# Kernel optimization log

Hardware: AMD Instinct MI355X
Metric: run time of the kernel (lower is better)

## Reference

```python
import jax, jax.numpy as jnp
import numpy as np

B, LQ, LK = 4, 4096, 4096
D = 1024          # num_heads * key_dim = 16 * 64
Q_DIM = 1024      # query_dim
K_DIM = 1024      # note: linear_k input dim; here inputs carry d_model features
V_DIM = 1024      # value_dim


def setup_inputs() -> dict:
    key = jax.random.key(0)
    ks = jax.random.split(key, 12)
    s_in = 1.0 / np.sqrt(Q_DIM)
    s_d = 1.0 / np.sqrt(D)
    return {
        "q": jax.random.normal(ks[0], (B, LQ, Q_DIM), jnp.float32),
        "k": jax.random.normal(ks[1], (B, LK, K_DIM), jnp.float32),
        "v": jax.random.normal(ks[2], (B, LK, V_DIM), jnp.float32),
        # Linear weights stored [in, out] so projection is x @ W + b
        "Wq": jax.random.normal(ks[3], (Q_DIM, D), jnp.float32) * s_in,
        "bq": jax.random.normal(ks[4], (D,), jnp.float32) * s_in,
        "Wk": jax.random.normal(ks[5], (K_DIM, D), jnp.float32) * s_in,
        "bk": jax.random.normal(ks[6], (D,), jnp.float32) * s_in,
        "Wv": jax.random.normal(ks[7], (V_DIM, D), jnp.float32) * s_in,
        "bv": jax.random.normal(ks[8], (D,), jnp.float32) * s_in,
        "Wo": jax.random.normal(ks[9], (D, V_DIM), jnp.float32) * s_d,
        "bo": jax.random.normal(ks[10], (V_DIM,), jnp.float32) * s_d,
    }


def reference(q, k, v, Wq, bq, Wk, bk, Wv, bv, Wo, bo):
    # Projections: [B, L, D]
    qp = jax.nn.softmax(q @ Wq + bq, axis=-1)   # softmax over feature dim
    kp = jax.nn.softmax(k @ Wk + bk, axis=-2)   # softmax over sequence dim
    vp = jax.nn.softmax(v @ Wv + bv, axis=-2)   # softmax over sequence dim
    # Dropout is identity in eval mode (module uses dropout_p at train only).
    scores = jnp.einsum("bqd,bkd->bqk", qp, kp)  # [B, LQ, LK]
    ctx = jnp.einsum("bqk,bkd->bqd", scores, vp)  # [B, LQ, D]
    return ctx @ Wo + bo                          # [B, LQ, V_DIM]
```

## Files before the change

kernel.cpp:

```cpp
#include <hip/hip_runtime.h>

typedef _Float16 f16x8 __attribute__((ext_vector_type(8)));
typedef float f32x4 __attribute__((ext_vector_type(4)));
typedef long lx2 __attribute__((ext_vector_type(2)));

__device__ __forceinline__ float h2f(unsigned short h) {
  return (float)__builtin_bit_cast(_Float16, h);
}
__device__ __forceinline__ unsigned short f2h(float f) {
  return __builtin_bit_cast(unsigned short, (_Float16)f);
}

#if __has_builtin(__builtin_amdgcn_cvt_pk_fp8_f32)
#define HW_FP8 1
#else
#define HW_FP8 0
#endif

__device__ __forceinline__ unsigned char f2e4_sw(float f) {
  unsigned short h = __builtin_bit_cast(unsigned short, (_Float16)f);
  unsigned s = (h >> 8) & 0x80u;
  unsigned ae = h & 0x7FFFu;
  if (ae >= 0x5F00u) return (unsigned char)(s | 0x7Eu);
  if (ae >= 0x2400u) {
    unsigned t = ae - 0x2000u;
    t = (t + 0x3Fu + ((t >> 7) & 1u)) >> 7;
    return (unsigned char)(s | t);
  }
  float v = (float)__builtin_bit_cast(_Float16, (unsigned short)ae) * 512.0f;
  int n = (int)rintf(v);
  return (unsigned char)(s | (unsigned)n);
}

__device__ __forceinline__ unsigned pk2e4(float a, float b) {
#if HW_FP8
  return (unsigned)__builtin_amdgcn_cvt_pk_fp8_f32(a, b, 0, false) & 0xFFFFu;
#else
  return (unsigned)f2e4_sw(a) | ((unsigned)f2e4_sw(b) << 8);
#endif
}
__device__ __forceinline__ unsigned pk4e4(float a, float b, float c, float d) {
#if HW_FP8
  int lo = __builtin_amdgcn_cvt_pk_fp8_f32(a, b, 0, false);
  return (unsigned)__builtin_amdgcn_cvt_pk_fp8_f32(c, d, lo, true);
#else
  return (unsigned)f2e4_sw(a) | ((unsigned)f2e4_sw(b) << 8) |
         ((unsigned)f2e4_sw(c) << 16) | ((unsigned)f2e4_sw(d) << 24);
#endif
}

__device__ __forceinline__ void gload_lds16(const void* g, void* l) {
  __builtin_amdgcn_global_load_lds(
      (const __attribute__((address_space(1))) void*)g,
      (__attribute__((address_space(3))) void*)l, 16, 0, 0);
}

__global__ __launch_bounds__(512, 4) void proj3(
    const float* __restrict__ A0, const float* __restrict__ A1,
    const float* __restrict__ A2, const unsigned short* __restrict__ WTb,
    const float* __restrict__ b0, const float* __restrict__ b1,
    const float* __restrict__ b2, unsigned char* __restrict__ C0,
    unsigned char* __restrict__ C1, unsigned char* __restrict__ C2,
    float* __restrict__ s0, float* __restrict__ s1, float* __restrict__ s2)
{
  __shared__ alignas(16) unsigned char smem[49152];
  const int tid  = threadIdx.x;
  const int lane = tid & 63;
  const int wave = tid >> 6;
  const int waveM = wave >> 2;
  const int waveN = wave & 3;

  const int wg = (int)blockIdx.x;
  const int w  = (wg & 7) * 192 + (wg >> 3);
  const int z  = w / 512;
  const int wl = w - z * 512;
  const int x  = wl & 3;
  const int rem = wl >> 2;
  const int y  = rem & 31;
  const int bz = rem >> 5;

  const float* Af = (z == 0) ? A0 : (z == 1) ? A1 : A2;
  const float* bi = (z == 0) ? b0 : (z == 1) ? b1 : b2;
  unsigned char* Cp = (z == 0) ? C0 : (z == 1) ? C1 : C2;
  float* sums = (z == 0) ? s0 : (z == 1) ? s1 : s2;

  const int m0 = y * 128, n0 = x * 256;

  const int srow = tid >> 3;
  const int scol = ((tid * 16) & 127) ^ ((srow & 7) << 4);
  const char* BpR = (const char*)(WTb + (size_t)z * 1048576)
                    + (size_t)n0 * 2048 + (size_t)srow * 2048 + scol;
  const char* ApR32 = (const char*)Af + (size_t)bz * (4096L * 1024 * 4)
                      + (size_t)m0 * 4096 + (size_t)srow * 4096 + (size_t)scol * 2;
  const unsigned oA0 = (unsigned)tid * 16;

  int offA[4], offB[4];
  {
    const int q16 = (lane >> 4) << 4;
#pragma unroll
    for (int mi = 0; mi < 4; ++mi) {
      const int r = waveM * 64 + mi * 16 + (lane & 15);
      offA[mi] = r * 128 + (q16 ^ ((r & 7) << 4));
    }
#pragma unroll
    for (int ni = 0; ni < 4; ++ni) {
      const int r = waveN * 64 + ni * 16 + (lane & 15);
      offB[ni] = 16384 + r * 128 + (q16 ^ ((r & 7) << 4));
    }
  }

  f32x4 acc[4][4] = {};

  float4 pf0, pf1, pf2, pf3;
  {
    const char* sa = ApR32;
    const char* sb = sa + 4096 * 64;
    pf0 = *(const float4*)sa;  pf1 = *(const float4*)(sa + 16);
    pf2 = *(const float4*)sb;  pf3 = *(const float4*)(sb + 16);
  }

  for (int kt = 0; kt < 16; ++kt) {
    const size_t kb = (size_t)kt * 128;
    {
      unsigned short h0[8], h1[8];
      const float* fa0 = (const float*)&pf0; const float* fa1 = (const float*)&pf1;
      const float* fb0 = (const float*)&pf2; const float* fb1 = (const float*)&pf3;
#pragma unroll
      for (int e = 0; e < 4; ++e) {
        h0[e] = f2h(fa0[e]); h0[4 + e] = f2h(fa1[e]);
        h1[e] = f2h(fb0[e]); h1[4 + e] = f2h(fb1[e]);
      }
      *(uint4*)&smem[oA0]        = *(const uint4*)h0;
      *(uint4*)&smem[oA0 + 8192] = *(const uint4*)h1;
      if (kt + 1 < 16) {
        const char* sa = ApR32 + (size_t)(kt + 1) * 256;
        const char* sb = sa + 4096 * 64;
        pf0 = *(const float4*)sa;  pf1 = *(const float4*)(sa + 16);
        pf2 = *(const float4*)sb;  pf3 = *(const float4*)(sb + 16);
      }
    }
    gload_lds16(BpR + kb,                      smem + 16384 + oA0);
    gload_lds16(BpR + 2048 * 64 + kb,          smem + 16384 + oA0 + 8192);
    gload_lds16(BpR + 2048 * 128 + kb,         smem + 16384 + oA0 + 16384);
    gload_lds16(BpR + 2048 * 192 + kb,         smem + 16384 + oA0 + 24576);
    __syncthreads();
#pragma unroll
    for (int kk = 0; kk < 2; ++kk) {
      const int kx = kk << 6;
      f16x8 aF[4], bF[4];
#pragma unroll
      for (int mi = 0; mi < 4; ++mi) aF[mi] = *(const f16x8*)&smem[offA[mi] ^ kx];
#pragma unroll
      for (int ni = 0; ni < 4; ++ni) bF[ni] = *(const f16x8*)&smem[offB[ni] ^ kx];
#pragma unroll
      for (int mi = 0; mi < 4; ++mi)
#pragma unroll
        for (int ni = 0; ni < 4; ++ni)
          acc[mi][ni] = __builtin_amdgcn_mfma_f32_16x16x32_f16(aF[mi], bF[ni], acc[mi][ni], 0, 0, 0);
    }
    __syncthreads();
  }

  const int rb = (lane >> 4) * 4;
  const int cb_ = lane & 15;
  const long sC = 4096L * 1024;

  if (z == 0) {
#pragma unroll
    for (int m = 0; m < 4; ++m) {
      const int row0 = m0 + waveM * 64 + m * 16 + rb;
      float rs0 = 0, rs1 = 0, rs2 = 0, rs3 = 0;
#pragma unroll
      for (int n = 0; n < 4; ++n) {
        const int col = n0 + waveN * 64 + n * 16 + cb_;
        const float badd = bi[col];
        const float e0 = __expf(acc[m][n][0] + badd);
        const float e1 = __expf(acc[m][n][1] + badd);
        const float e2 = __expf(acc[m][n][2] + badd);
        const float e3 = __expf(acc[m][n][3] + badd);
        const unsigned p01 = pk2e4(e0 * 0.0625f, e1 * 0.0625f);
        const unsigned p23 = pk2e4(e2 * 0.0625f, e3 * 0.0625f);
        unsigned char* C8 = Cp + (long)bz * sC;
        C8[(size_t)(row0 + 0) * 1024 + col] = (unsigned char)(p01 & 0xff);
        C8[(size_t)(row0 + 1) * 1024 + col] = (unsigned char)((p01 >> 8) & 0xff);
        C8[(size_t)(row0 + 2) * 1024 + col] = (unsigned char)(p23 & 0xff);
        C8[(size_t)(row0 + 3) * 1024 + col] = (unsigned char)((p23 >> 8) & 0xff);
        rs0 += e0; rs1 += e1; rs2 += e2; rs3 += e3;
      }
#pragma unroll
      for (int off = 1; off <= 8; off <<= 1) {
        rs0 += __shfl_xor(rs0, off);
        rs1 += __shfl_xor(rs1, off);
        rs2 += __shfl_xor(rs2, off);
        rs3 += __shfl_xor(rs3, off);
      }
      if ((lane & 15) == 0) {
        float* s = sums + (size_t)bz * 4096 + row0;
        atomicAdd(s + 0, rs0);
        atomicAdd(s + 1, rs1);
        atomicAdd(s + 2, rs2);
        atomicAdd(s + 3, rs3);
      }
    }
  } else {
    float cs[4] = {0.f, 0.f, 0.f, 0.f};
#pragma unroll
    for (int m = 0; m < 4; ++m) {
      const int row0 = m0 + waveM * 64 + m * 16 + rb;
#pragma unroll
      for (int n = 0; n < 4; ++n) {
        const int col = n0 + waveN * 64 + n * 16 + cb_;
        const float badd = bi[col];
        float ev[4];
        float ls = 0.f;
#pragma unroll
        for (int r = 0; r < 4; ++r) {
          ev[r] = __expf(acc[m][n][r] + badd);
          ls += ev[r];
        }
        cs[n] += ls;
        *(unsigned*)(Cp + (long)bz * sC + ((size_t)col << 12) + row0) =
            pk4e4(ev[0] * 0.0625f, ev[1] * 0.0625f, ev[2] * 0.0625f, ev[3] * 0.0625f);
      }
    }
#pragma unroll
    for (int n = 0; n < 4; ++n) {
      cs[n] += __shfl_xor(cs[n], 16);
      cs[n] += __shfl_xor(cs[n], 32);
    }
    if (lane < 16) {
#pragma unroll
      for (int n = 0; n < 4; ++n) {
        const int col = n0 + waveN * 64 + n * 16 + lane;
        atomicAdd(sums + ((size_t)bz << 10) + col, cs[n]);
      }
    }
  }
}

template <int OUTMODE>
__global__ __launch_bounds__(512, 4) void gemm8(
    const unsigned char* __restrict__ A, const unsigned char* __restrict__ Bt,
    void* __restrict__ Cv, const float* __restrict__ bias,
    const float* __restrict__ sums,
    int N, int K, int ldk, int gx, int gy, int nsplit,
    long sA, long sB, long sC)
{
  __shared__ alignas(16) unsigned char smem[49152];
  const int tid  = threadIdx.x;
  const int lane = tid & 63;
  const int wave = tid >> 6;
  const int waveM = wave >> 2;
  const int waveN = wave & 3;

  const int nwg = (int)gridDim.x;
  const int cpx = nwg >> 3;
  const int wg  = (int)blockIdx.x;
  const int w   = (wg & 7) * cpx + (wg >> 3);
  const int x   = w % gx;
  const int rem = w / gx;
  const int y   = rem % gy;
  const int zt  = rem / gy;
  const int bz  = zt / nsplit;
  const int sp  = zt % nsplit;

  const int m0 = y * 128, n0 = x * 256;
  const size_t ldkB = (size_t)ldk;
  const size_t ldkB64 = ldkB * 64, ldkB128 = ldkB * 128;

  const int srow = tid >> 3;
  const int scol = ((tid * 16) & 127) ^ ((srow & 7) << 4);
  const char* ApR;
  const char* BpR;
  {
    const char* Ab = (const char*)A + (long)bz * sA + (long)sp * K + (size_t)m0 * ldkB;
    const char* Bb = (const char*)Bt + (long)bz * sB + (long)sp * K + (size_t)n0 * ldkB;
    ApR = Ab + (size_t)srow * ldkB + scol;
    BpR = Bb + (size_t)srow * ldkB + scol;
  }
  const unsigned oA0 = (unsigned)tid * 16;

  int offA[4], offB[4];
  {
    const int q16 = (lane >> 4) << 4;
#pragma unroll
    for (int mi = 0; mi < 4; ++mi) {
      const int r = waveM * 64 + mi * 16 + (lane & 15);
      offA[mi] = r * 128 + (q16 ^ ((r & 7) << 4));
    }
#pragma unroll
    for (int ni = 0; ni < 4; ++ni) {
      const int r = waveN * 64 + ni * 16 + (lane & 15);
      offB[ni] = 16384 + r * 128 + (q16 ^ ((r & 7) << 4));
    }
  }

  f32x4 acc[4][4] = {};

  const int nk = K >> 7;
  for (int kt = 0; kt < nk; ++kt) {
    const size_t kb = (size_t)kt * 128;
    gload_lds16(ApR + kb,                     smem + oA0);
    gload_lds16(ApR + ldkB64 + kb,            smem + oA0 + 8192);
    gload_lds16(BpR + kb,                     smem + 16384 + oA0);
    gload_lds16(BpR + ldkB64 + kb,            smem + 16384 + oA0 + 8192);
    gload_lds16(BpR + ldkB128 + kb,           smem + 16384 + oA0 + 16384);
    gload_lds16(BpR + ldkB128 + ldkB64 + kb,  smem + 16384 + oA0 + 24576);
    __syncthreads();
#pragma unroll
    for (int kk = 0; kk < 2; ++kk) {
      const int kx = kk << 6;
      lx2 aF[4], bF[4];
#pragma unroll
      for (int mi = 0; mi < 4; ++mi) aF[mi] = *(const lx2*)&smem[offA[mi] ^ kx];
#pragma unroll
      for (int ni = 0; ni < 4; ++ni) bF[ni] = *(const lx2*)&smem[offB[ni] ^ kx];
#pragma unroll
      for (int h = 0; h < 2; ++h)
#pragma unroll
        for (int mi = 0; mi < 4; ++mi)
#pragma unroll
          for (int ni = 0; ni < 4; ++ni)
            acc[mi][ni] = __builtin_amdgcn_mfma_f32_16x16x32_fp8_fp8(
                aF[mi][h], bF[ni][h], acc[mi][ni], 0, 0, 0);
    }
    __syncthreads();
  }

  const int rb = (lane >> 4) * 4;
  const int cb_ = lane & 15;
  const long zout = (OUTMODE == 2) ? (long)zt : (long)bz;
#pragma unroll
  for (int m = 0; m < 4; ++m) {
    const int row0 = m0 + waveM * 64 + m * 16 + rb;
    float i0 = 0, i1 = 0, i2 = 0, i3 = 0;
    if (OUTMODE == 5) {
      const float4 s4 = *(const float4*)&sums[(size_t)zout * 4096 + row0];
      i0 = 1.0f / (256.0f * s4.x); i1 = 1.0f / (256.0f * s4.y);
      i2 = 1.0f / (256.0f * s4.z); i3 = 1.0f / (256.0f * s4.w);
    }
#pragma unroll
    for (int n = 0; n < 4; ++n) {
      const int col = n0 + waveN * 64 + n * 16 + cb_;
      if (OUTMODE == 2) {
#pragma unroll
        for (int r = 0; r < 4; ++r)
          ((unsigned short*)Cv)[zout * sC + (size_t)(row0 + r) * N + col] = f2h(acc[m][n][r]);
      } else {
        const float badd = bias[col];
        float* C32 = (float*)Cv;
        C32[zout * sC + (size_t)(row0 + 0) * N + col] = acc[m][n][0] * i0 + badd;
        C32[zout * sC + (size_t)(row0 + 1) * N + col] = acc[m][n][1] * i1 + badd;
        C32[zout * sC + (size_t)(row0 + 2) * N + col] = acc[m][n][2] * i2 + badd;
        C32[zout * sC + (size_t)(row0 + 3) * N + col] = acc[m][n][3] * i3 + badd;
      }
    }
  }
}

__global__ __launch_bounds__(256) void w_trh4(
    const float* __restrict__ W0, const float* __restrict__ W1,
    const float* __restrict__ W2, const float* __restrict__ W3,
    unsigned short* __restrict__ WTb, unsigned char* __restrict__ WoT8)
{
  __shared__ unsigned short tile[64][73];
  const int z = blockIdx.z;
  const float* W = (z == 0) ? W0 : (z == 1) ? W1 : (z == 2) ? W2 : W3;
  unsigned short* WT = WTb + (size_t)z * 1024 * 1024;
  const int c0 = blockIdx.x * 64;
  const int r0 = blockIdx.y * 64;
  const int tid = threadIdx.x;
  const int r = tid >> 2;
  const int cq = (tid & 3) * 16;
#pragma unroll
  for (int i = 0; i < 4; ++i) {
    const int c = cq + i * 4;
    const float4 v = *(const float4*)&W[(size_t)(r0 + r) * 1024 + c0 + c];
    tile[r][c + 0] = f2h(v.x);
    tile[r][c + 1] = f2h(v.y);
    tile[r][c + 2] = f2h(v.z);
    tile[r][c + 3] = f2h(v.w);
  }
  __syncthreads();
  const int c = tid >> 2;
  const int rq = (tid & 3) * 16;
  unsigned short outv[16];
#pragma unroll
  for (int j = 0; j < 16; ++j) outv[j] = tile[rq + j][c];
  unsigned short* Tb = WT + (size_t)(c0 + c) * 1024 + r0 + rq;
  ((uint4*)Tb)[0] = ((const uint4*)outv)[0];
  ((uint4*)Tb)[1] = ((const uint4*)outv)[1];
  if (z == 3) {
    unsigned u4[4];
#pragma unroll
    for (int j = 0; j < 4; ++j)
      u4[j] = pk4e4(h2f(outv[4 * j + 0]) * 8.f, h2f(outv[4 * j + 1]) * 8.f,
                    h2f(outv[4 * j + 2]) * 8.f, h2f(outv[4 * j + 3]) * 8.f);
    *(uint4*)(WoT8 + (size_t)(c0 + c) * 1024 + r0 + rq) = *(const uint4*)u4;
  }
}

__global__ __launch_bounds__(256) void red4m(
    const unsigned short* __restrict__ P, const float* __restrict__ skr,
    const float* __restrict__ svr, unsigned char* __restrict__ O)
{
  const int i = blockIdx.x * 256 + threadIdx.x;
  const int b = i >> 18;
  const int j = i & 262143;
  const int dk = j >> 8;
  const int dv0 = (j & 255) << 2;
  float s0 = 0, s1 = 0, s2 = 0, s3 = 0;
#pragma unroll
  for (int sl = 0; sl < 4; ++sl) {
    const uint2 u = *(const uint2*)(P + (((long)(b * 4 + sl)) << 20) + ((long)j << 2));
    s0 += h2f(u.x & 0xffff); s1 += h2f(u.x >> 16);
    s2 += h2f(u.y & 0xffff); s3 += h2f(u.y >> 16);
  }
  const float fk = 4194304.0f / skr[(b << 10) + dk];
  const float4 fv = *(const float4*)&svr[(b << 10) + dv0];
  ((unsigned*)O)[i] = pk4e4(s0 * fk / fv.x, s1 * fk / fv.y,
                            s2 * fk / fv.z, s3 * fk / fv.w);
}

__global__ __launch_bounds__(256) void red4g(
    const unsigned short* __restrict__ P, unsigned char* __restrict__ O)
{
  const int i = blockIdx.x * 256 + threadIdx.x;
  const int b = i >> 18;
  const int j = i & 262143;
  float s0 = 0, s1 = 0, s2 = 0, s3 = 0;
#pragma unroll
  for (int sl = 0; sl < 4; ++sl) {
    const uint2 u = *(const uint2*)(P + (((long)(b * 4 + sl)) << 20) + ((long)j << 2));
    s0 += h2f(u.x & 0xffff); s1 += h2f(u.x >> 16);
    s2 += h2f(u.y & 0xffff); s3 += h2f(u.y >> 16);
  }
  ((unsigned*)O)[i] = pk4e4(s0 * 0.03125f, s1 * 0.03125f,
                            s2 * 0.03125f, s3 * 0.03125f);
}

extern "C" void kernel_launch(void* const* d_in, const int* in_sizes, int n_in,
                              void* d_out, int out_size, void* d_ws, size_t ws_size,
                              hipStream_t stream) {
  const float* q  = (const float*)d_in[0];
  const float* k  = (const float*)d_in[1];
  const float* v  = (const float*)d_in[2];
  const float* Wq = (const float*)d_in[3];
  const float* bq = (const float*)d_in[4];
  const float* Wk = (const float*)d_in[5];
  const float* bk = (const float*)d_in[6];
  const float* Wv = (const float*)d_in[7];
  const float* bv = (const float*)d_in[8];
  const float* Wo = (const float*)d_in[9];
  const float* bo = (const float*)d_in[10];
  float* out = (float*)d_out;

  char* p = (char*)d_ws;
  unsigned short* Part = (unsigned short*)p; p += 33554432;
  unsigned short* WTb  = (unsigned short*)p; p += 8388608;
  unsigned char* WoT8 = (unsigned char*)p;   p += 1048576;
  unsigned char* Eq8  = (unsigned char*)p;   p += 16777216;
  unsigned char* ETk8 = (unsigned char*)p;   p += 16777216;
  unsigned char* ETv8 = (unsigned char*)p;   p += 16777216;
  unsigned char* Mh8  = (unsigned char*)p;   p += 4194304;
  unsigned char* GT8  = (unsigned char*)p;   p += 4194304;
  float* sqraw = (float*)p; p += 16384 * 4;
  float* skraw = (float*)p; p += 4096 * 4;
  float* svraw = (float*)p; p += 4096 * 4;

  const dim3 blk(256);
  const dim3 blk512(512);
  const long S22 = 4096L * 1024;
  const long S20 = 1024L * 1024;

  hipMemsetAsync(sqraw, 0, (16384 + 4096 + 4096) * sizeof(float), stream);

  w_trh4<<<dim3(16, 16, 4), blk, 0, stream>>>(Wq, Wk, Wv, Wo, WTb, WoT8);

  proj3<<<1536, blk512, 0, stream>>>(q, k, v, WTb, bq, bk, bv,
                                     Eq8, ETk8, ETv8, sqraw, skraw, svraw);

  gemm8<2><<<512, blk512, 0, stream>>>(ETk8, ETv8, Part, nullptr, nullptr,
      1024, 1024, 4096, 4, 8, 4, S22, S22, S20);
  red4m<<<4096, blk, 0, stream>>>(Part, skraw, svraw, Mh8);

  gemm8<2><<<512, blk512, 0, stream>>>(WoT8, Mh8, Part, nullptr, nullptr,
      1024, 256, 1024, 4, 8, 4, 0, S20, S20);
  red4g<<<4096, blk, 0, stream>>>(Part, GT8);

  gemm8<5><<<512, blk512, 0, stream>>>(Eq8, GT8, out, bo, sqraw,
      1024, 1024, 1024, 4, 32, 1, S22, S20, S22);

  (void)in_sizes; (void)n_in; (void)out_size; (void)ws_size;
}
```

Baseline: 263.0 us.

## Switch projection GEMM inputs and weights from fp16 to fp8 MFMA

The projection kernel now converts the fp32 activations and the transposed weights to fp8 e4m3, with the weights prescaled by 8. It runs fp8 MFMA over half as many K-tiles of 128 bytes, and the epilogue rescales the accumulator by 1/8. The weight-transpose kernel now writes one fp8 buffer for all four weights, which halves weight traffic and drops the separate fp16 copy. This cuts LDS and global bytes and doubles MFMA throughput per byte, at the cost of lower precision in the projection before the softmax.

```diff
diff --git a/kernel.cpp b/kernel.cpp
--- a/kernel.cpp
+++ b/kernel.cpp
@@ -1,6 +1,5 @@
 #include <hip/hip_runtime.h>
 
-typedef _Float16 f16x8 __attribute__((ext_vector_type(8)));
 typedef float f32x4 __attribute__((ext_vector_type(4)));
 typedef long lx2 __attribute__((ext_vector_type(2)));
 
@@ -32,13 +31,6 @@
   return (unsigned char)(s | (unsigned)n);
 }
 
-__device__ __forceinline__ unsigned pk2e4(float a, float b) {
-#if HW_FP8
-  return (unsigned)__builtin_amdgcn_cvt_pk_fp8_f32(a, b, 0, false) & 0xFFFFu;
-#else
-  return (unsigned)f2e4_sw(a) | ((unsigned)f2e4_sw(b) << 8);
-#endif
-}
 __device__ __forceinline__ unsigned pk4e4(float a, float b, float c, float d) {
 #if HW_FP8
   int lo = __builtin_amdgcn_cvt_pk_fp8_f32(a, b, 0, false);
@@ -48,6 +40,13 @@
          ((unsigned)f2e4_sw(c) << 16) | ((unsigned)f2e4_sw(d) << 24);
 #endif
 }
+__device__ __forceinline__ unsigned pk2e4(float a, float b) {
+#if HW_FP8
+  return (unsigned)__builtin_amdgcn_cvt_pk_fp8_f32(a, b, 0, false) & 0xFFFFu;
+#else
+  return (unsigned)f2e4_sw(a) | ((unsigned)f2e4_sw(b) << 8);
+#endif
+}
 
 __device__ __forceinline__ void gload_lds16(const void* g, void* l) {
   __builtin_amdgcn_global_load_lds(
@@ -57,7 +56,7 @@
 
 __global__ __launch_bounds__(512, 4) void proj3(
     const float* __restrict__ A0, const float* __restrict__ A1,
-    const float* __restrict__ A2, const unsigned short* __restrict__ WTb,
+    const float* __restrict__ A2, const unsigned char* __restrict__ WT8b,
     const float* __restrict__ b0, const float* __restrict__ b1,
     const float* __restrict__ b2, unsigned char* __restrict__ C0,
     unsigned char* __restrict__ C1, unsigned char* __restrict__ C2,
@@ -88,10 +87,10 @@
 
   const int srow = tid >> 3;
   const int scol = ((tid * 16) & 127) ^ ((srow & 7) << 4);
-  const char* BpR = (const char*)(WTb + (size_t)z * 1048576)
-                    + (size_t)n0 * 2048 + (size_t)srow * 2048 + scol;
-  const char* ApR32 = (const char*)Af + (size_t)bz * (4096L * 1024 * 4)
-                      + (size_t)m0 * 4096 + (size_t)srow * 4096 + (size_t)scol * 2;
+  const unsigned char* BpR = WT8b + ((size_t)z << 20)
+                             + (size_t)(n0 + srow) * 1024 + scol;
+  const float* ApR = Af + (size_t)bz * (4096L * 1024)
+                     + (size_t)(m0 + srow) * 1024 + scol;
   const unsigned oA0 = (unsigned)tid * 16;
 
   int offA[4], offB[4];
@@ -111,52 +110,54 @@
 
   f32x4 acc[4][4] = {};
 
-  float4 pf0, pf1, pf2, pf3;
-  {
-    const char* sa = ApR32;
-    const char* sb = sa + 4096 * 64;
-    pf0 = *(const float4*)sa;  pf1 = *(const float4*)(sa + 16);
-    pf2 = *(const float4*)sb;  pf3 = *(const float4*)(sb + 16);
-  }
-
-  for (int kt = 0; kt < 16; ++kt) {
+  float4 pa[4], pb[4];
+#pragma unroll
+  for (int j = 0; j < 4; ++j) {
+    pa[j] = *(const float4*)(ApR + j * 4);
+    pb[j] = *(const float4*)(ApR + 64 * 1024 + j * 4);
+  }
+
+  for (int kt = 0; kt < 8; ++kt) {
+    {
+      unsigned ua[4], ub[4];
+#pragma unroll
+      for (int j = 0; j < 4; ++j) {
+        ua[j] = pk4e4(pa[j].x, pa[j].y, pa[j].z, pa[j].w);
+        ub[j] = pk4e4(pb[j].x, pb[j].y, pb[j].z, pb[j].w);
+      }
+      *(uint4*)&smem[oA0]        = *(const uint4*)ua;
+      *(uint4*)&smem[oA0 + 8192] = *(const uint4*)ub;
+      if (kt + 1 < 8) {
+        const float* s = ApR + (size_t)(kt + 1) * 128;
+#pragma unroll
+        for (int j = 0; j < 4; ++j) {
+          pa[j] = *(const float4*)(s + j * 4);
+          pb[j] = *(const float4*)(s + 64 * 1024 + j * 4);
+        }
+      }
+    }
     const size_t kb = (size_t)kt * 128;
-    {
-      unsigned short h0[8], h1[8];
-      const float* fa0 = (const float*)&pf0; const float* fa1 = (const float*)&pf1;
-      const float* fb0 = (const float*)&pf2; const float* fb1 = (const float*)&pf3;
-#pragma unroll
-      for (int e = 0; e < 4; ++e) {
-        h0[e] = f2h(fa0[e]); h0[4 + e] = f2h(fa1[e]);
-        h1[e] = f2h(fb0[e]); h1[4 + e] = f2h(fb1[e]);
-      }
-      *(uint4*)&smem[oA0]        = *(const uint4*)h0;
-      *(uint4*)&smem[oA0 + 8192] = *(const uint4*)h1;
-      if (kt + 1 < 16) {
-        const char* sa = ApR32 + (size_t)(kt + 1) * 256;
-        const char* sb = sa + 4096 * 64;
-        pf0 = *(const float4*)sa;  pf1 = *(const float4*)(sa + 16);
-        pf2 = *(const float4*)sb;  pf3 = *(const float4*)(sb + 16);
-      }
-    }
-    gload_lds16(BpR + kb,                      smem + 16384 + oA0);
-    gload_lds16(BpR + 2048 * 64 + kb,          smem + 16384 + oA0 + 8192);
-    gload_lds16(BpR + 2048 * 128 + kb,         smem + 16384 + oA0 + 16384);
-    gload_lds16(BpR + 2048 * 192 + kb,         smem + 16384 + oA0 + 24576);
+    gload_lds16(BpR + kb,              smem + 16384 + oA0);
+    gload_lds16(BpR + 64 * 1024 + kb,  smem + 16384 + oA0 + 8192);
+    gload_lds16(BpR + 128 * 1024 + kb, smem + 16384 + oA0 + 16384);
+    gload_lds16(BpR + 192 * 1024 + kb, smem + 16384 + oA0 + 24576);
     __syncthreads();
 #pragma unroll
     for (int kk = 0; kk < 2; ++kk) {
       const int kx = kk << 6;
-      f16x8 aF[4], bF[4];
-#pragma unroll
-      for (int mi = 0; mi < 4; ++mi) aF[mi] = *(const f16x8*)&smem[offA[mi] ^ kx];
-#pragma unroll
-      for (int ni = 0; ni < 4; ++ni) bF[ni] = *(const f16x8*)&smem[offB[ni] ^ kx];
-#pragma unroll
-      for (int mi = 0; mi < 4; ++mi)
-#pragma unroll
-        for (int ni = 0; ni < 4; ++ni)
-          acc[mi][ni] = __builtin_amdgcn_mfma_f32_16x16x32_f16(aF[mi], bF[ni], acc[mi][ni], 0, 0, 0);
+      lx2 aF[4], bF[4];
+#pragma unroll
+      for (int mi = 0; mi < 4; ++mi) aF[mi] = *(const lx2*)&smem[offA[mi] ^ kx];
+#pragma unroll
+      for (int ni = 0; ni < 4; ++ni) bF[ni] = *(const lx2*)&smem[offB[ni] ^ kx];
+#pragma unroll
+      for (int h = 0; h < 2; ++h)
+#pragma unroll
+        for (int mi = 0; mi < 4; ++mi)
+#pragma unroll
+          for (int ni = 0; ni < 4; ++ni)
+            acc[mi][ni] = __builtin_amdgcn_mfma_f32_16x16x32_fp8_fp8(
+                aF[mi][h], bF[ni][h], acc[mi][ni], 0, 0, 0);
     }
     __syncthreads();
   }
@@ -174,10 +175,10 @@
       for (int n = 0; n < 4; ++n) {
         const int col = n0 + waveN * 64 + n * 16 + cb_;
         const float badd = bi[col];
-        const float e0 = __expf(acc[m][n][0] + badd);
-        const float e1 = __expf(acc[m][n][1] + badd);
-        const float e2 = __expf(acc[m][n][2] + badd);
-        const float e3 = __expf(acc[m][n][3] + badd);
+        const float e0 = __expf(acc[m][n][0] * 0.125f + badd);
+        const float e1 = __expf(acc[m][n][1] * 0.125f + badd);
+        const float e2 = __expf(acc[m][n][2] * 0.125f + badd);
+        const float e3 = __expf(acc[m][n][3] * 0.125f + badd);
         const unsigned p01 = pk2e4(e0 * 0.0625f, e1 * 0.0625f);
         const unsigned p23 = pk2e4(e2 * 0.0625f, e3 * 0.0625f);
         unsigned char* C8 = Cp + (long)bz * sC;
@@ -215,7 +216,7 @@
         float ls = 0.f;
 #pragma unroll
         for (int r = 0; r < 4; ++r) {
-          ev[r] = __expf(acc[m][n][r] + badd);
+          ev[r] = __expf(acc[m][n][r] * 0.125f + badd);
           ls += ev[r];
         }
         cs[n] += ls;
@@ -358,15 +359,15 @@
   }
 }
 
-__global__ __launch_bounds__(256) void w_trh4(
+__global__ __launch_bounds__(256) void w_tr8(
     const float* __restrict__ W0, const float* __restrict__ W1,
     const float* __restrict__ W2, const float* __restrict__ W3,
-    unsigned short* __restrict__ WTb, unsigned char* __restrict__ WoT8)
+    unsigned char* __restrict__ WT8b)
 {
-  __shared__ unsigned short tile[64][73];
+  __shared__ float tile[64][65];
   const int z = blockIdx.z;
   const float* W = (z == 0) ? W0 : (z == 1) ? W1 : (z == 2) ? W2 : W3;
-  unsigned short* WT = WTb + (size_t)z * 1024 * 1024;
+  unsigned char* WT8 = WT8b + ((size_t)z << 20);
   const int c0 = blockIdx.x * 64;
   const int r0 = blockIdx.y * 64;
   const int tid = threadIdx.x;
@@ -376,28 +377,20 @@
   for (int i = 0; i < 4; ++i) {
     const int c = cq + i * 4;
     const float4 v = *(const float4*)&W[(size_t)(r0 + r) * 1024 + c0 + c];
-    tile[r][c + 0] = f2h(v.x);
-    tile[r][c + 1] = f2h(v.y);
-    tile[r][c + 2] = f2h(v.z);
-    tile[r][c + 3] = f2h(v.w);
+    tile[r][c + 0] = v.x;
+    tile[r][c + 1] = v.y;
+    tile[r][c + 2] = v.z;
+    tile[r][c + 3] = v.w;
   }
   __syncthreads();
   const int c = tid >> 2;
   const int rq = (tid & 3) * 16;
-  unsigned short outv[16];
-#pragma unroll
-  for (int j = 0; j < 16; ++j) outv[j] = tile[rq + j][c];
-  unsigned short* Tb = WT + (size_t)(c0 + c) * 1024 + r0 + rq;
-  ((uint4*)Tb)[0] = ((const uint4*)outv)[0];
-  ((uint4*)Tb)[1] = ((const uint4*)outv)[1];
-  if (z == 3) {
-    unsigned u4[4];
-#pragma unroll
-    for (int j = 0; j < 4; ++j)
-      u4[j] = pk4e4(h2f(outv[4 * j + 0]) * 8.f, h2f(outv[4 * j + 1]) * 8.f,
-                    h2f(outv[4 * j + 2]) * 8.f, h2f(outv[4 * j + 3]) * 8.f);
-    *(uint4*)(WoT8 + (size_t)(c0 + c) * 1024 + r0 + rq) = *(const uint4*)u4;
-  }
+  unsigned u4[4];
+#pragma unroll
+  for (int j = 0; j < 4; ++j)
+    u4[j] = pk4e4(tile[rq + 4 * j + 0][c] * 8.f, tile[rq + 4 * j + 1][c] * 8.f,
+                  tile[rq + 4 * j + 2][c] * 8.f, tile[rq + 4 * j + 3][c] * 8.f);
+  *(uint4*)(WT8 + (size_t)(c0 + c) * 1024 + r0 + rq) = *(const uint4*)u4;
 }
 
 __global__ __launch_bounds__(256) void red4m(
@@ -457,8 +450,7 @@
 
   char* p = (char*)d_ws;
   unsigned short* Part = (unsigned short*)p; p += 33554432;
-  unsigned short* WTb  = (unsigned short*)p; p += 8388608;
-  unsigned char* WoT8 = (unsigned char*)p;   p += 1048576;
+  unsigned char* WT8b = (unsigned char*)p;   p += 4194304;
   unsigned char* Eq8  = (unsigned char*)p;   p += 16777216;
   unsigned char* ETk8 = (unsigned char*)p;   p += 16777216;
   unsigned char* ETv8 = (unsigned char*)p;   p += 16777216;
@@ -475,16 +467,16 @@
 
   hipMemsetAsync(sqraw, 0, (16384 + 4096 + 4096) * sizeof(float), stream);
 
-  w_trh4<<<dim3(16, 16, 4), blk, 0, stream>>>(Wq, Wk, Wv, Wo, WTb, WoT8);
-
-  proj3<<<1536, blk512, 0, stream>>>(q, k, v, WTb, bq, bk, bv,
+  w_tr8<<<dim3(16, 16, 4), blk, 0, stream>>>(Wq, Wk, Wv, Wo, WT8b);
+
+  proj3<<<1536, blk512, 0, stream>>>(q, k, v, WT8b, bq, bk, bv,
                                      Eq8, ETk8, ETv8, sqraw, skraw, svraw);
 
   gemm8<2><<<512, blk512, 0, stream>>>(ETk8, ETv8, Part, nullptr, nullptr,
       1024, 1024, 4096, 4, 8, 4, S22, S22, S20);
   red4m<<<4096, blk, 0, stream>>>(Part, skraw, svraw, Mh8);
 
-  gemm8<2><<<512, blk512, 0, stream>>>(WoT8, Mh8, Part, nullptr, nullptr,
+  gemm8<2><<<512, blk512, 0, stream>>>(WT8b + (3L << 20), Mh8, Part, nullptr, nullptr,
       1024, 256, 1024, 4, 8, 4, 0, S20, S20);
   red4g<<<4096, blk, 0, stream>>>(Part, GT8);
 
```

Result: slower. 280.8 us (+6.8%).
